# Kernel tuning notes

Measured on AMD Instinct MI355X. Metric: run time of the kernel, lower is better.

The kernel has to match this reference:

```python
import jax, jax.numpy as jnp
import numpy as np

C = 256
NUM_HEADS = 8
EPS = 1e-5


def setup_inputs() -> dict:
    key = jax.random.key(0)
    ks = jax.random.split(key, 8)
    x = jax.random.normal(ks[0], (2, C, 64, 64), dtype=jnp.float32)
    # LayerNorm params (torch default: weight=1, bias=0)
    norm_w = jnp.ones((C,), jnp.float32)
    norm_b = jnp.zeros((C,), jnp.float32)
    # qkv Linear: weight (3C, C), bias (3C,)
    qkv_w = jax.random.normal(ks[1], (3 * C, C), dtype=jnp.float32) * (1.0 / np.sqrt(C))
    qkv_b = jax.random.normal(ks[2], (3 * C,), dtype=jnp.float32) * 0.01
    # proj Linear: weight (C, C), bias (C,)
    proj_w = jax.random.normal(ks[3], (C, C), dtype=jnp.float32) * (1.0 / np.sqrt(C))
    proj_b = jax.random.normal(ks[4], (C,), dtype=jnp.float32) * 0.01
    # gamma initialized to zeros in torch, but use small nonzero so output depends on attention
    gamma = jnp.full((1,), 0.1, jnp.float32)
    return {"x": x, "norm_w": norm_w, "norm_b": norm_b, "qkv_w": qkv_w,
            "qkv_b": qkv_b, "proj_w": proj_w, "proj_b": proj_b, "gamma": gamma}


def reference(x, norm_w, norm_b, qkv_w, qkv_b, proj_w, proj_b, gamma):
    B, Cc, H, W = x.shape
    N = H * W
    nh = NUM_HEADS
    hd = Cc // nh
    scale = hd ** (-0.5)

    # (B, N, C)
    x_flat = x.reshape(B, Cc, N).transpose(0, 2, 1)

    # LayerNorm over last dim
    mu = jnp.mean(x_flat, axis=-1, keepdims=True)
    var = jnp.mean(jnp.square(x_flat - mu), axis=-1, keepdims=True)
    x_norm = (x_flat - mu) * jax.lax.rsqrt(var + EPS) * norm_w + norm_b

    # QKV projection: (B, N, 3C) -> (3, B, nh, N, hd)
    qkv = x_norm @ qkv_w.T + qkv_b
    qkv = qkv.reshape(B, N, 3, nh, hd).transpose(2, 0, 3, 1, 4)
    q, k, v = qkv[0], qkv[1], qkv[2]

    # attention scores (B, nh, N, N); note torch code scales AFTER q@k.T
    attn = jnp.einsum('bhnd,bhmd->bhnm', q, k) * scale
    attn = jax.nn.softmax(attn, axis=-1)

    # (B, nh, N, hd) -> (B, N, C)
    x_attn = jnp.einsum('bhnm,bhmd->bhnd', attn, v)
    x_attn = x_attn.transpose(0, 2, 1, 3).reshape(B, N, Cc)
    x_attn = x_attn @ proj_w.T + proj_b

    # back to (B, C, H, W) and scaled residual
    x_attn = x_attn.transpose(0, 2, 1).reshape(B, Cc, H, W)
    return gamma * x_attn + x
```

## Files before the change

kernel.cpp:

```cpp
#include <hip/hip_runtime.h>

#define CCH   256
#define NSEQ  4096
#define NH    8
#define HD    32

typedef short s8x __attribute__((ext_vector_type(8)));
typedef float f4x __attribute__((ext_vector_type(4)));

__device__ __forceinline__ f4x mfma16(s8x a, s8x b, f4x c) {
  return __builtin_amdgcn_mfma_f32_16x16x32_bf16(a, b, c, 0, 0, 0);
}

__device__ __forceinline__ unsigned short f2bf(float f) {
  union { float f; unsigned int u; } v; v.f = f;
  unsigned int u = v.u + 0x7fffu + ((v.u >> 16) & 1u);
  return (unsigned short)(u >> 16);
}

__device__ __forceinline__ unsigned int pk_bf_rnd(float lo, float hi) {
  return (unsigned int)f2bf(lo) | ((unsigned int)f2bf(hi) << 16);
}

__device__ __forceinline__ unsigned int pk_bf_trunc(float lo, float hi) {
  union { float f; unsigned int u; } a, b; a.f = lo; b.f = hi;
  return __builtin_amdgcn_perm(b.u, a.u, 0x07060302);
}

#if defined(__has_builtin)
#if __has_builtin(__builtin_amdgcn_exp2f)
#define FEXP2(x) __builtin_amdgcn_exp2f(x)
#endif
#endif
#ifndef FEXP2
__device__ __forceinline__ float __fexp2_asm(float x) {
  float r; asm("v_exp_f32 %0, %1" : "=v"(r) : "v"(x)); return r;
}
#define FEXP2(x) __fexp2_asm(x)
#endif

#define C2SCALE (0.17677669529663689f * 1.4426950408889634f)

__global__ __launch_bounds__(256) void ln_cvt_kernel(const float* __restrict__ x,
                                                     const float* __restrict__ nw,
                                                     const float* __restrict__ nb,
                                                     unsigned short* __restrict__ xn,
                                                     const float* __restrict__ qw,
                                                     const float* __restrict__ pw,
                                                     unsigned short* __restrict__ qwb,
                                                     unsigned short* __restrict__ pwb) {
  if (blockIdx.x >= 256) {
    const int t = (blockIdx.x - 256) * 256 + threadIdx.x;
    const float4* src;
    unsigned short* dst;
    int idx;
    if (t < 49152) { src = reinterpret_cast<const float4*>(qw); dst = qwb; idx = t; }
    else           { src = reinterpret_cast<const float4*>(pw); dst = pwb; idx = t - 49152; }
    const float4 vv = src[idx];
    union { unsigned short u[4]; uint2 v; } pk;
    pk.u[0] = f2bf(vv.x); pk.u[1] = f2bf(vv.y); pk.u[2] = f2bf(vv.z); pk.u[3] = f2bf(vv.w);
    *reinterpret_cast<uint2*>(dst + 4 * idx) = pk.v;
    return;
  }

  __shared__ float Ls[256 * 32];
  __shared__ float Sred[2][32][8];
  __shared__ float Mrs[32][2];
  const int t  = threadIdx.x;
  const int n  = t & 31;
  const int cg = t >> 5;
  const int p0 = blockIdx.x * 32;
  const int b  = p0 >> 12;
  const int n0 = p0 & 4095;
  const float* xb = x + (size_t)b * CCH * NSEQ + n0;

  #pragma unroll
  for (int i = 0; i < 32; ++i) {
    const int c = i * 8 + cg;
    Ls[c * 32 + (n ^ (c & 31))] = xb[(size_t)c * NSEQ + n];
  }
  __syncthreads();

  float s = 0.f, sq = 0.f;
  #pragma unroll
  for (int j = 0; j < 32; ++j) {
    const int c = cg * 32 + j;
    const float v = Ls[c * 32 + (n ^ j)];
    s += v; sq += v * v;
  }
  Sred[0][n][cg] = s; Sred[1][n][cg] = sq;
  __syncthreads();
  float ts = 0.f, tq = 0.f;
  #pragma unroll
  for (int g = 0; g < 8; ++g) { ts += Sred[0][n][g]; tq += Sred[1][n][g]; }
  const float mean = ts * (1.f / 256.f);
  const float rstd = rsqrtf(tq * (1.f / 256.f) - mean * mean + 1e-5f);
  if (cg == 0) { Mrs[n][0] = mean; Mrs[n][1] = rstd; }
  __syncthreads();

  const int n2  = t >> 3;
  const int c8b = t & 7;
  const float mean2 = Mrs[n2][0];
  const float rstd2 = Mrs[n2][1];
  unsigned short* orow = xn + ((size_t)b * NSEQ + n0 + n2) * CCH;
  #pragma unroll
  for (int j8 = 0; j8 < 4; ++j8) {
    const int cb = (j8 * 8 + c8b) * 8;
    unsigned int w_[4];
    #pragma unroll
    for (int hw = 0; hw < 4; ++hw) {
      const int c = cb + hw * 2;
      const float v0 = Ls[c * 32 + (n2 ^ (c & 31))];
      const float v1 = Ls[(c + 1) * 32 + (n2 ^ ((c + 1) & 31))];
      const float y0 = (v0 - mean2) * rstd2 * nw[c] + nb[c];
      const float y1 = (v1 - mean2) * rstd2 * nw[c + 1] + nb[c + 1];
      w_[hw] = pk_bf_rnd(y0, y1);
    }
    uint4 pkv; pkv.x = w_[0]; pkv.y = w_[1]; pkv.z = w_[2]; pkv.w = w_[3];
    *reinterpret_cast<uint4*>(orow + cb) = pkv;
  }
}

__global__ __launch_bounds__(256, 6) void qkv_gemm(const unsigned short* __restrict__ xn,
                                                   const unsigned short* __restrict__ w,
                                                   const float* __restrict__ bias,
                                                   unsigned short* __restrict__ q,
                                                   unsigned short* __restrict__ k,
                                                   unsigned short* __restrict__ vt) {
  __shared__ unsigned short As[64 * 64];
  __shared__ unsigned short Bs[64 * 64];
  const int tid = threadIdx.x;
  const int wv  = tid >> 6;
  const int lane = tid & 63;
  const int quad = lane >> 4, l16 = lane & 15;
  const int mt = blockIdx.x;
  const int nt = blockIdx.y;

  f4x acc[4];
  #pragma unroll
  for (int ni = 0; ni < 4; ++ni)
    acc[ni] = (f4x){0.f, 0.f, 0.f, 0.f};

  for (int kb = 0; kb < 4; ++kb) {
    if (kb) __syncthreads();
    #pragma unroll
    for (int j = 0; j < 2; ++j) {
      const int c = j * 256 + tid;
      const int ar = c >> 3, acr = c & 7;
      *reinterpret_cast<s8x*>(&As[ar * 64 + ((acr ^ (ar & 7)) << 3)]) =
        *reinterpret_cast<const s8x*>(xn + (size_t)(mt * 64 + ar) * CCH + kb * 64 + acr * 8);
    }
    #pragma unroll
    for (int j = 0; j < 2; ++j) {
      const int c = j * 256 + tid;
      const int br = c >> 3, bcr = c & 7;
      *reinterpret_cast<s8x*>(&Bs[br * 64 + ((bcr ^ (br & 7)) << 3)]) =
        *reinterpret_cast<const s8x*>(w + (size_t)(nt * 64 + br) * CCH + kb * 64 + bcr * 8);
    }
    __syncthreads();
    #pragma unroll
    for (int kin = 0; kin < 2; ++kin) {
      const int chx = ((kin * 4 + quad) ^ (l16 & 7)) << 3;
      const s8x a0 = *reinterpret_cast<const s8x*>(&As[(wv * 16 + l16) * 64 + chx]);
      #pragma unroll
      for (int ni = 0; ni < 4; ++ni) {
        const s8x bf = *reinterpret_cast<const s8x*>(&Bs[(ni * 16 + l16) * 64 + chx]);
        acc[ni] = mfma16(a0, bf, acc[ni]);
      }
    }
  }

  const int sel = nt >> 2;
  #pragma unroll
  for (int ni = 0; ni < 4; ++ni) {
    const int o = nt * 64 + ni * 16 + l16;
    const float bs = bias[o];
    const int ol = o & 255;
    const int head = ol >> 5, d = ol & 31;
    const int g0 = mt * 64 + wv * 16 + quad * 4;
    const int bb = g0 >> 12, n0 = g0 & 4095;
    if (sel == 2) {
      unsigned short* vp = vt + ((size_t)(bb * NH + head) * HD + d) * NSEQ + n0;
      uint2 pk;
      pk.x = pk_bf_rnd(acc[ni][0] + bs, acc[ni][1] + bs);
      pk.y = pk_bf_rnd(acc[ni][2] + bs, acc[ni][3] + bs);
      *reinterpret_cast<uint2*>(vp) = pk;
    } else {
      const float sc = (sel == 0) ? C2SCALE : 1.f;
      unsigned short* base = (sel == 0) ? q : k;
      #pragma unroll
      for (int r = 0; r < 4; ++r)
        base[((size_t)(bb * NH + head) * NSEQ + n0 + r) * HD + d] = f2bf((acc[ni][r] + bs) * sc);
    }
  }
}

__global__ __launch_bounds__(256, 6) void proj_gemm(const unsigned short* __restrict__ xa,
                                                    const unsigned short* __restrict__ w,
                                                    const float* __restrict__ bias,
                                                    const float* __restrict__ gamma,
                                                    const float* __restrict__ x,
                                                    float* __restrict__ out) {
  __shared__ unsigned short As[64 * 64];
  __shared__ unsigned short Bs[32 * 64];
  const int tid = threadIdx.x;
  const int wv  = tid >> 6;
  const int lane = tid & 63;
  const int quad = lane >> 4, l16 = lane & 15;
  const int mt = blockIdx.x;
  const int nt = blockIdx.y;

  f4x acc[2];
  acc[0] = (f4x){0.f, 0.f, 0.f, 0.f};
  acc[1] = (f4x){0.f, 0.f, 0.f, 0.f};

  for (int kb = 0; kb < 4; ++kb) {
    if (kb) __syncthreads();
    #pragma unroll
    for (int j = 0; j < 2; ++j) {
      const int c = j * 256 + tid;
      const int ar = c >> 3, acr = c & 7;
      *reinterpret_cast<s8x*>(&As[ar * 64 + ((acr ^ (ar & 7)) << 3)]) =
        *reinterpret_cast<const s8x*>(xa + (size_t)(mt * 64 + ar) * CCH + kb * 64 + acr * 8);
    }
    {
      const int c = tid;
      const int br = c >> 3, bcr = c & 7;
      *reinterpret_cast<s8x*>(&Bs[br * 64 + ((bcr ^ (br & 7)) << 3)]) =
        *reinterpret_cast<const s8x*>(w + (size_t)(nt * 32 + br) * CCH + kb * 64 + bcr * 8);
    }
    __syncthreads();
    #pragma unroll
    for (int kin = 0; kin < 2; ++kin) {
      const int chx = ((kin * 4 + quad) ^ (l16 & 7)) << 3;
      const s8x a0 = *reinterpret_cast<const s8x*>(&As[(wv * 16 + l16) * 64 + chx]);
      #pragma unroll
      for (int ni = 0; ni < 2; ++ni) {
        const s8x bf = *reinterpret_cast<const s8x*>(&Bs[(ni * 16 + l16) * 64 + chx]);
        acc[ni] = mfma16(a0, bf, acc[ni]);
      }
    }
  }

  const float g0 = gamma[0];
  #pragma unroll
  for (int ni = 0; ni < 2; ++ni) {
    const int c = nt * 32 + ni * 16 + l16;
    const float bs = bias[c];
    const int gr = mt * 64 + wv * 16 + quad * 4;
    const int bb = gr >> 12, n0 = gr & 4095;
    const size_t off = (size_t)(bb * CCH + c) * NSEQ + n0;
    const float4 xv = *reinterpret_cast<const float4*>(x + off);
    float4 ov;
    ov.x = g0 * (acc[ni][0] + bs) + xv.x;
    ov.y = g0 * (acc[ni][1] + bs) + xv.y;
    ov.z = g0 * (acc[ni][2] + bs) + xv.z;
    ov.w = g0 * (acc[ni][3] + bs) + xv.w;
    *reinterpret_cast<float4*>(out + off) = ov;
  }
}

__global__ __launch_bounds__(256, 4) void fa_kernel(const unsigned short* __restrict__ q,
                                                    const unsigned short* __restrict__ k,
                                                    const unsigned short* __restrict__ vt,
                                                    float* __restrict__ Opart,
                                                    float* __restrict__ Lpart) {
  __shared__ unsigned short Ks[2][64 * 40];
  __shared__ unsigned short Vs[2][32 * 72];
  __shared__ unsigned short Ps[128 * 72];

  const int tid  = threadIdx.x;
  const int wv   = tid >> 6;
  const int lane = tid & 63;
  const int quad = lane >> 4;
  const int l16  = lane & 15;
  const int i    = blockIdx.x;
  const int bh   = i & 15;
  const int rest = i >> 4;
  const int half = rest & 1;
  const int qblk = rest >> 1;
  const int kv0  = half * 2048;

  const unsigned short* kb_ = k  + ((size_t)bh * NSEQ + kv0) * HD;
  const unsigned short* vb_ = vt + (size_t)bh * HD * NSEQ + kv0;

  const int krow = tid >> 2;
  const int kdc  = (tid & 3) * 8;
  const int vrow = tid >> 3;
  const int vkc  = (tid & 7) * 8;

  s8x bq0, bq1;
  {
    const unsigned short* qb = q + ((size_t)bh * NSEQ + (size_t)qblk * 128 + wv * 32) * HD;
    bq0 = *reinterpret_cast<const s8x*>(qb + (size_t)l16 * HD + quad * 8);
    bq1 = *reinterpret_cast<const s8x*>(qb + (size_t)(16 + l16) * HD + quad * 8);
  }

  uint4 kreg = *reinterpret_cast<const uint4*>(kb_ + (size_t)krow * HD + kdc);
  uint4 vreg = *reinterpret_cast<const uint4*>(vb_ + (size_t)vrow * NSEQ + vkc);
  *reinterpret_cast<uint4*>(&Ks[0][krow * 40 + kdc]) = kreg;
  *reinterpret_cast<uint4*>(&Vs[0][vrow * 72 + vkc]) = vreg;
  kreg = *reinterpret_cast<const uint4*>(kb_ + (size_t)(64 + krow) * HD + kdc);
  vreg = *reinterpret_cast<const uint4*>(vb_ + (size_t)vrow * NSEQ + 64 + vkc);
  __syncthreads();

  f4x st[4][2];
  #pragma unroll
  for (int ii = 0; ii < 4; ++ii) {
    const s8x ak = *reinterpret_cast<const s8x*>(&Ks[0][(ii * 16 + l16) * 40 + quad * 8]);
    const f4x z = {0.f, 0.f, 0.f, 0.f};
    st[ii][0] = mfma16(ak, bq0, z);
    st[ii][1] = mfma16(ak, bq1, z);
  }

  f4x oacc[2][2];
  #pragma unroll
  for (int dt = 0; dt < 2; ++dt)
    #pragma unroll
    for (int ct = 0; ct < 2; ++ct)
      oacc[dt][ct] = (f4x){0.f, 0.f, 0.f, 0.f};
  f4x accL[2] = {(f4x){0.f, 0.f, 0.f, 0.f}, (f4x){0.f, 0.f, 0.f, 0.f}};

  s8x ones;
  #pragma unroll
  for (int j = 0; j < 8; ++j) ones[j] = (short)0x3F80;

  const int r0 = (wv * 32 + l16) * 72;
  const int r1 = (wv * 32 + 16 + l16) * 72;

  s8x vavr[4];

  for (int t = 0; t < 32; ++t) {
    const int c = t & 1;

    s8x bp[4];
    if (t > 0) {
      bp[0] = *reinterpret_cast<const s8x*>(&Ps[r0 + 0 * 32 + quad * 8]);
      bp[1] = *reinterpret_cast<const s8x*>(&Ps[r1 + 0 * 32 + quad * 8]);
      bp[2] = *reinterpret_cast<const s8x*>(&Ps[r0 + 1 * 32 + quad * 8]);
      bp[3] = *reinterpret_cast<const s8x*>(&Ps[r1 + 1 * 32 + quad * 8]);
    }

    if (t + 1 < 32) {
      *reinterpret_cast<uint4*>(&Ks[c ^ 1][krow * 40 + kdc]) = kreg;
      *reinterpret_cast<uint4*>(&Vs[c ^ 1][vrow * 72 + vkc]) = vreg;
    }

    if (t > 0) {
      #pragma unroll
      for (int kb2 = 0; kb2 < 2; ++kb2) {
        oacc[0][0] = mfma16(vavr[kb2],     bp[2 * kb2],     oacc[0][0]);
        oacc[1][0] = mfma16(vavr[2 + kb2], bp[2 * kb2],     oacc[1][0]);
        oacc[0][1] = mfma16(vavr[kb2],     bp[2 * kb2 + 1], oacc[0][1]);
        oacc[1][1] = mfma16(vavr[2 + kb2], bp[2 * kb2 + 1], oacc[1][1]);
        accL[0] = mfma16(ones, bp[2 * kb2],     accL[0]);
        accL[1] = mfma16(ones, bp[2 * kb2 + 1], accL[1]);
      }
    }

    #pragma unroll
    for (int ct = 0; ct < 2; ++ct) {
      const int prow = (wv * 32 + ct * 16 + l16) * 72;
      #pragma unroll
      for (int ii = 0; ii < 4; ++ii) {
        const float e0 = FEXP2(st[ii][ct][0]);
        const float e1 = FEXP2(st[ii][ct][1]);
        const float e2 = FEXP2(st[ii][ct][2]);
        const float e3 = FEXP2(st[ii][ct][3]);
        uint2 pw;
        pw.x = pk_bf_trunc(e0, e1);
        pw.y = pk_bf_trunc(e2, e3);
        *reinterpret_cast<uint2*>(&Ps[prow + ii * 16 + quad * 4]) = pw;
      }
    }

    if (t + 2 < 32) {
      kreg = *reinterpret_cast<const uint4*>(kb_ + (size_t)((t + 2) * 64 + krow) * HD + kdc);
      vreg = *reinterpret_cast<const uint4*>(vb_ + (size_t)vrow * NSEQ + (t + 2) * 64 + vkc);
    }

    #pragma unroll
    for (int kb2 = 0; kb2 < 2; ++kb2) {
      vavr[kb2]     = *reinterpret_cast<const s8x*>(&Vs[c][l16 * 72 + kb2 * 32 + quad * 8]);
      vavr[2 + kb2] = *reinterpret_cast<const s8x*>(&Vs[c][(16 + l16) * 72 + kb2 * 32 + quad * 8]);
    }

    __syncthreads();

    if (t + 1 < 32) {
      #pragma unroll
      for (int ii = 0; ii < 4; ++ii) {
        const s8x ak = *reinterpret_cast<const s8x*>(&Ks[c ^ 1][(ii * 16 + l16) * 40 + quad * 8]);
        const f4x z = {0.f, 0.f, 0.f, 0.f};
        st[ii][0] = mfma16(ak, bq0, z);
        st[ii][1] = mfma16(ak, bq1, z);
      }
    }
  }

  {
    s8x bp[4];
    bp[0] = *reinterpret_cast<const s8x*>(&Ps[r0 + 0 * 32 + quad * 8]);
    bp[1] = *reinterpret_cast<const s8x*>(&Ps[r1 + 0 * 32 + quad * 8]);
    bp[2] = *reinterpret_cast<const s8x*>(&Ps[r0 + 1 * 32 + quad * 8]);
    bp[3] = *reinterpret_cast<const s8x*>(&Ps[r1 + 1 * 32 + quad * 8]);
    #pragma unroll
    for (int kb2 = 0; kb2 < 2; ++kb2) {
      oacc[0][0] = mfma16(vavr[kb2],     bp[2 * kb2],     oacc[0][0]);
      oacc[1][0] = mfma16(vavr[2 + kb2], bp[2 * kb2],     oacc[1][0]);
      oacc[0][1] = mfma16(vavr[kb2],     bp[2 * kb2 + 1], oacc[0][1]);
      oacc[1][1] = mfma16(vavr[2 + kb2], bp[2 * kb2 + 1], oacc[1][1]);
      accL[0] = mfma16(ones, bp[2 * kb2],     accL[0]);
      accL[1] = mfma16(ones, bp[2 * kb2 + 1], accL[1]);
    }
  }

  #pragma unroll
  for (int ct = 0; ct < 2; ++ct) {
    const int qg = qblk * 128 + wv * 32 + ct * 16 + l16;
    float* obase = Opart + ((size_t)(half * 16 + bh) * NSEQ + qg) * HD;
    #pragma unroll
    for (int dt = 0; dt < 2; ++dt) {
      float4 ov;
      ov.x = oacc[dt][ct][0]; ov.y = oacc[dt][ct][1];
      ov.z = oacc[dt][ct][2]; ov.w = oacc[dt][ct][3];
      *reinterpret_cast<float4*>(obase + dt * 16 + quad * 4) = ov;
    }
    if (quad == 0)
      Lpart[(size_t)(half * 16 + bh) * NSEQ + qg] = accL[ct][0];
  }
}

__global__ __launch_bounds__(256) void fa_combine(const float* __restrict__ Opart,
                                                  const float* __restrict__ Lpart,
                                                  unsigned short* __restrict__ xa) {
  const int t  = blockIdx.x * 256 + threadIdx.x;
  const int c8 = t & 3;
  const int n  = (t >> 2) & 4095;
  const int bh = t >> 14;
  const int b  = bh >> 3, h = bh & 7;

  const size_t o0 = ((size_t)bh * NSEQ + n) * HD + c8 * 8;
  const size_t o1 = o0 + (size_t)16 * NSEQ * HD;
  const float4 a0 = *reinterpret_cast<const float4*>(Opart + o0);
  const float4 a1 = *reinterpret_cast<const float4*>(Opart + o0 + 4);
  const float4 b0 = *reinterpret_cast<const float4*>(Opart + o1);
  const float4 b1 = *reinterpret_cast<const float4*>(Opart + o1 + 4);
  const float l0 = Lpart[(size_t)bh * NSEQ + n];
  const float l1 = Lpart[(size_t)(16 + bh) * NSEQ + n];
  const float rl = 1.f / (l0 + l1);

  uint4 ow;
  ow.x = pk_bf_rnd((a0.x + b0.x) * rl, (a0.y + b0.y) * rl);
  ow.y = pk_bf_rnd((a0.z + b0.z) * rl, (a0.w + b0.w) * rl);
  ow.z = pk_bf_rnd((a1.x + b1.x) * rl, (a1.y + b1.y) * rl);
  ow.w = pk_bf_rnd((a1.z + b1.z) * rl, (a1.w + b1.w) * rl);
  *reinterpret_cast<uint4*>(xa + ((size_t)b * NSEQ + n) * CCH + h * HD + c8 * 8) = ow;
}

extern "C" void kernel_launch(void* const* d_in, const int* in_sizes, int n_in,
                              void* d_out, int out_size, void* d_ws, size_t ws_size,
                              hipStream_t stream) {
  const float* x      = (const float*)d_in[0];
  const float* norm_w = (const float*)d_in[1];
  const float* norm_b = (const float*)d_in[2];
  const float* qkv_w  = (const float*)d_in[3];
  const float* qkv_b  = (const float*)d_in[4];
  const float* proj_w = (const float*)d_in[5];
  const float* proj_b = (const float*)d_in[6];
  const float* gamma  = (const float*)d_in[7];
  float* out = (float*)d_out;

  char* ws = (char*)d_ws;
  unsigned short* xn  = (unsigned short*)(ws);
  unsigned short* qwb = (unsigned short*)(ws + 4194304);
  unsigned short* pwb = (unsigned short*)(ws + 4587520);
  unsigned short* q   = (unsigned short*)(ws + 4718592);
  unsigned short* k   = (unsigned short*)(ws + 8912896);
  unsigned short* vt  = (unsigned short*)(ws + 13107200);
  unsigned short* xa  = (unsigned short*)(ws + 17301504);
  float* Opart        = (float*)(ws + 21495808);
  float* Lpart        = (float*)(ws + 38273024);

  hipLaunchKernelGGL(ln_cvt_kernel, dim3(512), dim3(256), 0, stream,
                     x, norm_w, norm_b, xn, qkv_w, proj_w, qwb, pwb);
  hipLaunchKernelGGL(qkv_gemm,  dim3(128, 12), dim3(256), 0, stream, xn, qwb, qkv_b, q, k, vt);
  hipLaunchKernelGGL(fa_kernel, dim3(1024), dim3(256), 0, stream, q, k, vt, Opart, Lpart);
  hipLaunchKernelGGL(fa_combine, dim3(1024), dim3(256), 0, stream, Opart, Lpart, xa);
  hipLaunchKernelGGL(proj_gemm, dim3(128, 8), dim3(256), 0, stream, xa, pwb, proj_b, gamma, x, out);
}
```

Before: 147.1 us.

## Store K, V and P tiles in LDS pre-arranged as MFMA fragments

```diff
diff --git a/kernel.cpp b/kernel.cpp
--- a/kernel.cpp
+++ b/kernel.cpp
@@ -265,9 +265,9 @@
                                                     const unsigned short* __restrict__ vt,
                                                     float* __restrict__ Opart,
                                                     float* __restrict__ Lpart) {
-  __shared__ unsigned short Ks[2][64 * 40];
-  __shared__ unsigned short Vs[2][32 * 72];
-  __shared__ unsigned short Ps[128 * 72];
+  __shared__ unsigned short Kf[2][2048];
+  __shared__ unsigned short Vf[2][2048];
+  __shared__ unsigned short Pf[8192];
 
   const int tid  = threadIdx.x;
   const int wv   = tid >> 6;
@@ -284,10 +284,10 @@
   const unsigned short* kb_ = k  + ((size_t)bh * NSEQ + kv0) * HD;
   const unsigned short* vb_ = vt + (size_t)bh * HD * NSEQ + kv0;
 
-  const int krow = tid >> 2;
-  const int kdc  = (tid & 3) * 8;
-  const int vrow = tid >> 3;
-  const int vkc  = (tid & 7) * 8;
+  const int kfrow = (tid >> 6) * 16 + (tid & 15);
+  const int kfcol = ((tid >> 4) & 3) * 8;
+  const int vfrow = ((tid >> 7) & 1) * 16 + (tid & 15);
+  const int vfcol = ((tid >> 6) & 1) * 32 + ((tid >> 4) & 3) * 8;
 
   s8x bq0, bq1;
   {
@@ -296,18 +296,18 @@
     bq1 = *reinterpret_cast<const s8x*>(qb + (size_t)(16 + l16) * HD + quad * 8);
   }
 
-  uint4 kreg = *reinterpret_cast<const uint4*>(kb_ + (size_t)krow * HD + kdc);
-  uint4 vreg = *reinterpret_cast<const uint4*>(vb_ + (size_t)vrow * NSEQ + vkc);
-  *reinterpret_cast<uint4*>(&Ks[0][krow * 40 + kdc]) = kreg;
-  *reinterpret_cast<uint4*>(&Vs[0][vrow * 72 + vkc]) = vreg;
-  kreg = *reinterpret_cast<const uint4*>(kb_ + (size_t)(64 + krow) * HD + kdc);
-  vreg = *reinterpret_cast<const uint4*>(vb_ + (size_t)vrow * NSEQ + 64 + vkc);
+  uint4 kreg = *reinterpret_cast<const uint4*>(kb_ + (size_t)kfrow * HD + kfcol);
+  uint4 vreg = *reinterpret_cast<const uint4*>(vb_ + (size_t)vfrow * NSEQ + vfcol);
+  *reinterpret_cast<uint4*>(&Kf[0][tid * 8]) = kreg;
+  *reinterpret_cast<uint4*>(&Vf[0][tid * 8]) = vreg;
+  kreg = *reinterpret_cast<const uint4*>(kb_ + (size_t)(64 + kfrow) * HD + kfcol);
+  vreg = *reinterpret_cast<const uint4*>(vb_ + (size_t)vfrow * NSEQ + 64 + vfcol);
   __syncthreads();
 
   f4x st[4][2];
   #pragma unroll
   for (int ii = 0; ii < 4; ++ii) {
-    const s8x ak = *reinterpret_cast<const s8x*>(&Ks[0][(ii * 16 + l16) * 40 + quad * 8]);
+    const s8x ak = *reinterpret_cast<const s8x*>(&Kf[0][(ii * 64 + lane) * 8]);
     const f4x z = {0.f, 0.f, 0.f, 0.f};
     st[ii][0] = mfma16(ak, bq0, z);
     st[ii][1] = mfma16(ak, bq1, z);
@@ -325,8 +325,7 @@
   #pragma unroll
   for (int j = 0; j < 8; ++j) ones[j] = (short)0x3F80;
 
-  const int r0 = (wv * 32 + l16) * 72;
-  const int r1 = (wv * 32 + 16 + l16) * 72;
+  const int pbase = wv * 4 * 64 * 8;
 
   s8x vavr[4];
 
@@ -335,15 +334,14 @@
 
     s8x bp[4];
     if (t > 0) {
-      bp[0] = *reinterpret_cast<const s8x*>(&Ps[r0 + 0 * 32 + quad * 8]);
-      bp[1] = *reinterpret_cast<const s8x*>(&Ps[r1 + 0 * 32 + quad * 8]);
-      bp[2] = *reinterpret_cast<const s8x*>(&Ps[r0 + 1 * 32 + quad * 8]);
-      bp[3] = *reinterpret_cast<const s8x*>(&Ps[r1 + 1 * 32 + quad * 8]);
+      #pragma unroll
+      for (int j = 0; j < 4; ++j)
+        bp[j] = *reinterpret_cast<const s8x*>(&Pf[pbase + (j * 64 + lane) * 8]);
     }
 
     if (t + 1 < 32) {
-      *reinterpret_cast<uint4*>(&Ks[c ^ 1][krow * 40 + kdc]) = kreg;
-      *reinterpret_cast<uint4*>(&Vs[c ^ 1][vrow * 72 + vkc]) = vreg;
+      *reinterpret_cast<uint4*>(&Kf[c ^ 1][tid * 8]) = kreg;
+      *reinterpret_cast<uint4*>(&Vf[c ^ 1][tid * 8]) = vreg;
     }
 
     if (t > 0) {
@@ -360,7 +358,6 @@
 
     #pragma unroll
     for (int ct = 0; ct < 2; ++ct) {
-      const int prow = (wv * 32 + ct * 16 + l16) * 72;
       #pragma unroll
       for (int ii = 0; ii < 4; ++ii) {
         const float e0 = FEXP2(st[ii][ct][0]);
@@ -370,27 +367,26 @@
         uint2 pw;
         pw.x = pk_bf_trunc(e0, e1);
         pw.y = pk_bf_trunc(e2, e3);
-        *reinterpret_cast<uint2*>(&Ps[prow + ii * 16 + quad * 4]) = pw;
+        const int paddr = pbase + (((ii >> 1) * 2 + ct) * 64 + ((ii & 1) * 2 + (quad >> 1)) * 16 + l16) * 8 + (quad & 1) * 4;
+        *reinterpret_cast<uint2*>(&Pf[paddr]) = pw;
       }
     }
 
     if (t + 2 < 32) {
-      kreg = *reinterpret_cast<const uint4*>(kb_ + (size_t)((t + 2) * 64 + krow) * HD + kdc);
-      vreg = *reinterpret_cast<const uint4*>(vb_ + (size_t)vrow * NSEQ + (t + 2) * 64 + vkc);
-    }
-
-    #pragma unroll
-    for (int kb2 = 0; kb2 < 2; ++kb2) {
-      vavr[kb2]     = *reinterpret_cast<const s8x*>(&Vs[c][l16 * 72 + kb2 * 32 + quad * 8]);
-      vavr[2 + kb2] = *reinterpret_cast<const s8x*>(&Vs[c][(16 + l16) * 72 + kb2 * 32 + quad * 8]);
-    }
+      kreg = *reinterpret_cast<const uint4*>(kb_ + (size_t)((t + 2) * 64 + kfrow) * HD + kfcol);
+      vreg = *reinterpret_cast<const uint4*>(vb_ + (size_t)vfrow * NSEQ + (t + 2) * 64 + vfcol);
+    }
+
+    #pragma unroll
+    for (int j = 0; j < 4; ++j)
+      vavr[j] = *reinterpret_cast<const s8x*>(&Vf[c][(j * 64 + lane) * 8]);
 
     __syncthreads();
 
     if (t + 1 < 32) {
       #pragma unroll
       for (int ii = 0; ii < 4; ++ii) {
-        const s8x ak = *reinterpret_cast<const s8x*>(&Ks[c ^ 1][(ii * 16 + l16) * 40 + quad * 8]);
+        const s8x ak = *reinterpret_cast<const s8x*>(&Kf[c ^ 1][(ii * 64 + lane) * 8]);
         const f4x z = {0.f, 0.f, 0.f, 0.f};
         st[ii][0] = mfma16(ak, bq0, z);
         st[ii][1] = mfma16(ak, bq1, z);
@@ -400,10 +396,9 @@
 
   {
     s8x bp[4];
-    bp[0] = *reinterpret_cast<const s8x*>(&Ps[r0 + 0 * 32 + quad * 8]);
-    bp[1] = *reinterpret_cast<const s8x*>(&Ps[r1 + 0 * 32 + quad * 8]);
-    bp[2] = *reinterpret_cast<const s8x*>(&Ps[r0 + 1 * 32 + quad * 8]);
-    bp[3] = *reinterpret_cast<const s8x*>(&Ps[r1 + 1 * 32 + quad * 8]);
+    #pragma unroll
+    for (int j = 0; j < 4; ++j)
+      bp[j] = *reinterpret_cast<const s8x*>(&Pf[pbase + (j * 64 + lane) * 8]);
     #pragma unroll
     for (int kb2 = 0; kb2 < 2; ++kb2) {
       oacc[0][0] = mfma16(vavr[kb2],     bp[2 * kb2],     oacc[0][0]);
```

Measured after the change: 143.8 us, median of 2. 1.02x faster.
